# Performance work log

Hardware: AMD Instinct MI355X
Metric: run time of the kernel (lower is better)

The kernel has to match this reference:

```python
import jax, jax.numpy as jnp
import numpy as np

NUM_HEADS = 12
LN_EPS = 1e-5


def _layernorm(t, w, b):
    # LayerNorm over last dim (head_dim), biased variance as in torch
    mu = jnp.mean(t, axis=-1, keepdims=True)
    var = jnp.mean(jnp.square(t - mu), axis=-1, keepdims=True)
    return (t - mu) * jax.lax.rsqrt(var + LN_EPS) * w + b


def _apply_rope(t, cos, sin):
    # t: [B, H, S, D]; cos/sin: [S, D//2]; interleaved complex pairs (torch view_as_complex)
    tr = t[..., 0::2]
    ti = t[..., 1::2]
    c = cos[None, None, :, :]
    s = sin[None, None, :, :]
    out_r = tr * c - ti * s
    out_i = tr * s + ti * c
    return jnp.stack([out_r, out_i], axis=-1).reshape(t.shape)


def setup_inputs() -> dict:
    key = jax.random.key(0)
    ks = jax.random.split(key, 6)
    B, N, C = 16, 1024, 768
    H = NUM_HEADS
    D = C // H  # 64
    P, L = 1, 32
    rot_len = N - P - L  # 991
    x = jax.random.normal(ks[0], (B, N, C), dtype=jnp.float32)
    # rotary frequencies (llama-style)
    inv_freq = 1.0 / (10000.0 ** (np.arange(0, D, 2, dtype=np.float32) / D))
    angles = np.arange(rot_len, dtype=np.float32)[:, None] * inv_freq[None, :]
    cos = jnp.asarray(np.cos(angles))
    sin = jnp.asarray(np.sin(angles))
    # parameters (qkv_bias=False, qk_norm=True)
    w_qkv = jax.random.normal(ks[1], (C, 3 * C), dtype=jnp.float32) * (C ** -0.5)
    q_ln_w = jnp.ones((D,), jnp.float32)
    q_ln_b = jnp.zeros((D,), jnp.float32)
    k_ln_w = jnp.ones((D,), jnp.float32)
    k_ln_b = jnp.zeros((D,), jnp.float32)
    w_proj = jax.random.normal(ks[2], (C, C), dtype=jnp.float32) * (C ** -0.5)
    b_proj = jnp.zeros((C,), jnp.float32)
    return {
        "x": x, "cos": cos, "sin": sin,
        "w_qkv": w_qkv,
        "q_ln_w": q_ln_w, "q_ln_b": q_ln_b,
        "k_ln_w": k_ln_w, "k_ln_b": k_ln_b,
        "w_proj": w_proj, "b_proj": b_proj,
        "num_prefix_tokens": 1, "num_latent_tokens": 32,
    }


def reference(x, cos, sin, w_qkv, q_ln_w, q_ln_b, k_ln_w, k_ln_b, w_proj, b_proj,
              num_prefix_tokens, num_latent_tokens):
    B, N, C = x.shape
    H = NUM_HEADS
    D = C // H
    P, L = num_prefix_tokens, num_latent_tokens
    scale = D ** -0.5

    qkv = (x @ w_qkv).reshape(B, N, 3, H, D)
    qkv = jnp.transpose(qkv, (2, 0, 3, 1, 4))  # [3, B, H, N, D]
    q, k, v = qkv[0], qkv[1], qkv[2]

    q = _layernorm(q, q_ln_w, q_ln_b)
    k = _layernorm(k, k_ln_w, k_ln_b)

    # partial RoPE: only the middle [P : N-L] tokens are rotated
    q_rot = _apply_rope(q[:, :, P:N - L], cos, sin)
    k_rot = _apply_rope(k[:, :, P:N - L], cos, sin)
    q = jnp.concatenate([q[:, :, :P], q_rot, q[:, :, N - L:]], axis=2)
    k = jnp.concatenate([k[:, :, :P], k_rot, k[:, :, N - L:]], axis=2)

    attn = jnp.einsum("bhqd,bhkd->bhqk", q * scale, k)
    attn = jax.nn.softmax(attn, axis=-1)
    out = jnp.einsum("bhqk,bhkd->bhqd", attn, v)
    out = jnp.transpose(out, (0, 2, 1, 3)).reshape(B, N, C)
    return out @ w_proj + b_proj
```

## Files before the change

kernel.cpp:

```cpp
#include <hip/hip_runtime.h>
#include <hip/hip_bf16.h>

typedef __attribute__((ext_vector_type(8))) short v8s;
typedef __attribute__((ext_vector_type(4))) short v4s;
typedef __attribute__((ext_vector_type(4))) float f32x4;

__device__ __forceinline__ float bf2f(short s){
  unsigned u = ((unsigned)(unsigned short)s) << 16;
  float f; __builtin_memcpy(&f, &u, 4); return f;
}
__device__ __forceinline__ short f2bf(float f){
  unsigned u; __builtin_memcpy(&u, &f, 4);
  unsigned r = (u + 0x7FFFu + ((u >> 16) & 1u)) >> 16;
  return (short)r;
}

__global__ __launch_bounds__(256) void k_cast8(const float* __restrict__ in,
                                               short* __restrict__ out, long n){
  long i = ((long)blockIdx.x * 256 + threadIdx.x) * 8;
  long stride = (long)gridDim.x * 256 * 8;
  for (; i < n; i += stride){
    float4 a = *(const float4*)(in + i);
    float4 b = *(const float4*)(in + i + 4);
    v8s v;
    v[0]=f2bf(a.x); v[1]=f2bf(a.y); v[2]=f2bf(a.z); v[3]=f2bf(a.w);
    v[4]=f2bf(b.x); v[5]=f2bf(b.y); v[6]=f2bf(b.z); v[7]=f2bf(b.w);
    *(v8s*)(out + i) = v;
  }
}

__global__ __launch_bounds__(256) void k_tcast(const float* __restrict__ in,
                                               short* __restrict__ out, int R, int Cc){
  __shared__ float T[32][33];
  int tx = threadIdx.x & 31, ty = threadIdx.x >> 5;
  int r0 = blockIdx.x * 32, c0 = blockIdx.y * 32;
  #pragma unroll
  for (int p = 0; p < 4; p++){
    int r = ty + p*8;
    T[r][tx] = in[(long)(r0 + r)*Cc + c0 + tx];
  }
  __syncthreads();
  #pragma unroll
  for (int p = 0; p < 4; p++){
    int r = ty + p*8;
    out[(long)(c0 + r)*R + r0 + tx] = f2bf(T[tx][r]);
  }
}

template<int OUT_MODE>
__global__ __launch_bounds__(256) void k_gemm(const short* __restrict__ A,
                                              const short* __restrict__ Bt,
                                              void* __restrict__ Cout,
                                              const float* __restrict__ bias,
                                              int M, int N, int K){
  __shared__ short As[128][72];
  __shared__ short Bs[128][72];
  int row0 = blockIdx.x * 128, col0 = blockIdx.y * 128;
  int t = threadIdx.x;
  int lane = t & 63, w = t >> 6;
  int g = lane >> 4, r16 = lane & 15;
  int wr = w >> 1, wc = w & 1;
  f32x4 acc[4][4];
  #pragma unroll
  for (int mi = 0; mi < 4; mi++)
    #pragma unroll
    for (int ni = 0; ni < 4; ni++)
      acc[mi][ni] = (f32x4){0.f,0.f,0.f,0.f};

  for (int kt = 0; kt < K; kt += 64){
    #pragma unroll
    for (int p = 0; p < 4; p++){
      int idx = t + p*256;
      int rr = idx >> 3, vc = idx & 7;
      *(v8s*)&As[rr][vc*8] = *(const v8s*)&A[(long)(row0 + rr)*K + kt + vc*8];
    }
    #pragma unroll
    for (int p = 0; p < 4; p++){
      int idx = t + p*256;
      int rr = idx >> 3, vc = idx & 7;
      *(v8s*)&Bs[rr][vc*8] = *(const v8s*)&Bt[(long)(col0 + rr)*K + kt + vc*8];
    }
    __syncthreads();
    #pragma unroll
    for (int ks = 0; ks < 2; ks++){
      v8s af[4], bfr[4];
      #pragma unroll
      for (int mi = 0; mi < 4; mi++)
        af[mi] = *(const v8s*)&As[wr*64 + mi*16 + r16][ks*32 + g*8];
      #pragma unroll
      for (int ni = 0; ni < 4; ni++)
        bfr[ni] = *(const v8s*)&Bs[wc*64 + ni*16 + r16][ks*32 + g*8];
      #pragma unroll
      for (int mi = 0; mi < 4; mi++)
        #pragma unroll
        for (int ni = 0; ni < 4; ni++)
          acc[mi][ni] = __builtin_amdgcn_mfma_f32_16x16x32_bf16(af[mi], bfr[ni], acc[mi][ni], 0, 0, 0);
    }
    __syncthreads();
  }
  #pragma unroll
  for (int mi = 0; mi < 4; mi++)
    #pragma unroll
    for (int ni = 0; ni < 4; ni++){
      int rbase = row0 + wr*64 + mi*16 + g*4;
      int cc = col0 + wc*64 + ni*16 + r16;
      #pragma unroll
      for (int j = 0; j < 4; j++){
        float v = acc[mi][ni][j];
        if (OUT_MODE == 0)
          ((short*)Cout)[(long)(rbase + j)*N + cc] = f2bf(v);
        else
          ((float*)Cout)[(long)(rbase + j)*N + cc] = v + bias[cc];
      }
    }
}

__global__ __launch_bounds__(256) void k_lnrope(const short* __restrict__ QKV,
     const float* __restrict__ cosT, const float* __restrict__ sinT,
     const float* __restrict__ qw, const float* __restrict__ qb,
     const float* __restrict__ kw, const float* __restrict__ kb,
     short* __restrict__ Qb, short* __restrict__ Kb, short* __restrict__ Vt){
  __shared__ short Vs[64][72];
  int blk = blockIdx.x;
  int ntile = blk & 15, h = (blk >> 4) % 12, b = blk / 192;
  int t = threadIdx.x;
  int tl = t >> 2, ch = t & 3;
  int n = ntile*64 + tl;
  long row = (long)(b*1024 + n) * 2304;
  int d0 = ch * 16;
  long outrow = ((long)(b*12 + h)*1024 + n) * 64;

  #pragma unroll
  for (int sel = 0; sel < 2; sel++){
    const short* src = &QKV[row + sel*768 + h*64 + d0];
    float f[16];
    v8s a0 = *(const v8s*)src;
    v8s a1 = *(const v8s*)(src + 8);
    #pragma unroll
    for (int i = 0; i < 8; i++){ f[i] = bf2f(a0[i]); f[8+i] = bf2f(a1[i]); }
    float s1 = 0.f, s2 = 0.f;
    #pragma unroll
    for (int i = 0; i < 16; i++){ s1 += f[i]; s2 += f[i]*f[i]; }
    s1 += __shfl_xor(s1, 1); s2 += __shfl_xor(s2, 1);
    s1 += __shfl_xor(s1, 2); s2 += __shfl_xor(s2, 2);
    float mu = s1 * (1.0f/64.0f);
    float var = s2 * (1.0f/64.0f) - mu*mu;
    float rs = rsqrtf(var + 1e-5f);
    const float* wp = sel ? kw : qw;
    const float* bp = sel ? kb : qb;
    #pragma unroll
    for (int i = 0; i < 16; i++) f[i] = (f[i] - mu)*rs*wp[d0+i] + bp[d0+i];
    if (n >= 1 && n < 992){
      int pos = n - 1;
      const float* cp = &cosT[pos*32 + ch*8];
      const float* sp = &sinT[pos*32 + ch*8];
      #pragma unroll
      for (int i = 0; i < 8; i++){
        float c = cp[i], s = sp[i];
        float tr = f[2*i], ti = f[2*i+1];
        f[2*i]   = tr*c - ti*s;
        f[2*i+1] = tr*s + ti*c;
      }
    }
    if (sel == 0){
      #pragma unroll
      for (int i = 0; i < 16; i++) f[i] *= 0.125f;
    }
    v8s o0, o1;
    #pragma unroll
    for (int i = 0; i < 8; i++){ o0[i] = f2bf(f[i]); o1[i] = f2bf(f[8+i]); }
    short* dst = sel ? &Kb[outrow + d0] : &Qb[outrow + d0];
    *(v8s*)dst = o0;
    *(v8s*)(dst + 8) = o1;
  }
  {
    const short* vsrc = &QKV[row + 1536 + h*64 + d0];
    *(v8s*)&Vs[tl][d0]     = *(const v8s*)vsrc;
    *(v8s*)&Vs[tl][d0 + 8] = *(const v8s*)(vsrc + 8);
  }
  __syncthreads();
  {
    int d = tl, nch = ch;
    v8s o0, o1;
    #pragma unroll
    for (int i = 0; i < 8; i++){ o0[i] = Vs[nch*16 + i][d]; o1[i] = Vs[nch*16 + 8 + i][d]; }
    long vrow = ((long)(b*12 + h)*64 + d)*1024 + ntile*64 + nch*16;
    *(v8s*)&Vt[vrow]     = o0;
    *(v8s*)&Vt[vrow + 8] = o1;
  }
}

__global__ __launch_bounds__(256) void k_attn(const short* __restrict__ Qb,
                                              const short* __restrict__ Kb,
                                              const short* __restrict__ Vt,
                                              short* __restrict__ O){
  __shared__ short Ks[64][72];
  __shared__ short Vts[64][72];
  int blk = blockIdx.x;
  int qt = blk & 15, h = (blk >> 4) % 12, b = blk / 192;
  long bh = b*12 + h;
  int t = threadIdx.x, lane = t & 63, w = t >> 6;
  int g = lane >> 4, r16 = lane & 15;
  int q0 = qt*64 + w*16;

  v8s bq[2];
  #pragma unroll
  for (int tt = 0; tt < 2; tt++)
    bq[tt] = *(const v8s*)&Qb[(bh*1024 + q0 + r16)*64 + tt*32 + g*8];

  f32x4 oacc[4];
  #pragma unroll
  for (int t2 = 0; t2 < 4; t2++) oacc[t2] = (f32x4){0.f,0.f,0.f,0.f};
  float m_run = -1e30f, l_run = 0.f;

  for (int kt = 0; kt < 1024; kt += 64){
    #pragma unroll
    for (int p = 0; p < 2; p++){
      int idx = t + p*256;
      int rr = idx >> 3, vc = idx & 7;
      *(v8s*)&Ks[rr][vc*8]  = *(const v8s*)&Kb[(bh*1024 + kt + rr)*64 + vc*8];
      *(v8s*)&Vts[rr][vc*8] = *(const v8s*)&Vt[(bh*64 + rr)*1024 + kt + vc*8];
    }
    __syncthreads();

    f32x4 sacc[4];
    #pragma unroll
    for (int f = 0; f < 4; f++) sacc[f] = (f32x4){0.f,0.f,0.f,0.f};
    #pragma unroll
    for (int tt = 0; tt < 2; tt++){
      #pragma unroll
      for (int f = 0; f < 4; f++){
        v8s ak = *(const v8s*)&Ks[f*16 + r16][tt*32 + g*8];
        sacc[f] = __builtin_amdgcn_mfma_f32_16x16x32_bf16(ak, bq[tt], sacc[f], 0, 0, 0);
      }
    }
    float mt = -1e30f;
    #pragma unroll
    for (int f = 0; f < 4; f++)
      #pragma unroll
      for (int j = 0; j < 4; j++) mt = fmaxf(mt, sacc[f][j]);
    mt = fmaxf(mt, __shfl_xor(mt, 16));
    mt = fmaxf(mt, __shfl_xor(mt, 32));
    float m_new = fmaxf(m_run, mt);
    float alpha = __expf(m_run - m_new);
    float p[4][4];
    float lsum = 0.f;
    #pragma unroll
    for (int f = 0; f < 4; f++)
      #pragma unroll
      for (int j = 0; j < 4; j++){
        p[f][j] = __expf(sacc[f][j] - m_new);
        lsum += p[f][j];
      }
    lsum += __shfl_xor(lsum, 16);
    lsum += __shfl_xor(lsum, 32);
    l_run = l_run*alpha + lsum;
    m_run = m_new;
    float aj4[4];
    #pragma unroll
    for (int j = 0; j < 4; j++) aj4[j] = __shfl(alpha, 4*g + j, 64);
    #pragma unroll
    for (int t2 = 0; t2 < 4; t2++)
      #pragma unroll
      for (int j = 0; j < 4; j++) oacc[t2][j] *= aj4[j];

    v8s pa[4];
    #pragma unroll
    for (int f = 0; f < 4; f++){
      #pragma unroll
      for (int j = 0; j < 4; j++) pa[f][j] = f2bf(p[f][j]);
      #pragma unroll
      for (int j = 4; j < 8; j++) pa[f][j] = 0;
    }
    #pragma unroll
    for (int t2 = 0; t2 < 4; t2++)
      #pragma unroll
      for (int f = 0; f < 4; f++){
        v4s v4 = *(const v4s*)&Vts[t2*16 + r16][f*16 + g*4];
        v8s bv;
        bv[0]=v4[0]; bv[1]=v4[1]; bv[2]=v4[2]; bv[3]=v4[3];
        bv[4]=0; bv[5]=0; bv[6]=0; bv[7]=0;
        oacc[t2] = __builtin_amdgcn_mfma_f32_16x16x32_bf16(pa[f], bv, oacc[t2], 0, 0, 0);
      }
    __syncthreads();
  }
  float linv = 1.0f / l_run;
  float lj[4];
  #pragma unroll
  for (int j = 0; j < 4; j++) lj[j] = __shfl(linv, 4*g + j, 64);
  #pragma unroll
  for (int t2 = 0; t2 < 4; t2++)
    #pragma unroll
    for (int j = 0; j < 4; j++){
      float v = oacc[t2][j] * lj[j];
      O[((long)b*1024 + q0 + 4*g + j)*768 + h*64 + t2*16 + r16] = f2bf(v);
    }
}

extern "C" void kernel_launch(void* const* d_in, const int* in_sizes, int n_in,
                              void* d_out, int out_size, void* d_ws, size_t ws_size,
                              hipStream_t stream) {
  const float* x      = (const float*)d_in[0];
  const float* cosT   = (const float*)d_in[1];
  const float* sinT   = (const float*)d_in[2];
  const float* w_qkv  = (const float*)d_in[3];
  const float* q_ln_w = (const float*)d_in[4];
  const float* q_ln_b = (const float*)d_in[5];
  const float* k_ln_w = (const float*)d_in[6];
  const float* k_ln_b = (const float*)d_in[7];
  const float* w_proj = (const float*)d_in[8];
  const float* b_proj = (const float*)d_in[9];

  char* ws = (char*)d_ws;
  short* Xb       = (short*)(ws);
  short* Wqkv_bt  = (short*)(ws + 25165824);
  short* Wproj_bt = (short*)(ws + 28704768);
  short* QKV      = (short*)(ws + 29884416);
  short* Qb       = (short*)(ws + 105381888);
  short* Kb       = (short*)(ws + 130547712);
  short* Vt       = (short*)(ws + 155713536);
  short* O        = (short*)(ws + 180879360);

  k_cast8<<<6144, 256, 0, stream>>>(x, Xb, 12582912L);
  k_tcast<<<dim3(24, 72), 256, 0, stream>>>(w_qkv, Wqkv_bt, 768, 2304);
  k_tcast<<<dim3(24, 24), 256, 0, stream>>>(w_proj, Wproj_bt, 768, 768);
  k_gemm<0><<<dim3(128, 18), 256, 0, stream>>>(Xb, Wqkv_bt, QKV, nullptr, 16384, 2304, 768);
  k_lnrope<<<3072, 256, 0, stream>>>(QKV, cosT, sinT, q_ln_w, q_ln_b, k_ln_w, k_ln_b, Qb, Kb, Vt);
  k_attn<<<3072, 256, 0, stream>>>(Qb, Kb, Vt, O);
  k_gemm<1><<<dim3(128, 6), 256, 0, stream>>>(O, Wproj_bt, d_out, b_proj, 16384, 768, 768);
}
```

Before: 420.2 us.

## Use direct global-to-LDS loads with XOR swizzle, exp2 softmax, larger attention blocks

GEMM and attention tiles are now loaded with global_load_lds straight into unpadded LDS. An XOR swizzle on the column index avoids bank conflicts, and the loads skip the register round trip. The Q scale folds in log2(e) so the softmax can use exp2f. Attention blocks grow to 512 threads with 128 queries each, so every K/V tile is reused by twice as many queries. The swizzle has to match the per-wave LDS destination layout of global_load_lds exactly, and the larger blocks may reduce occupancy.

```diff
diff --git a/kernel.cpp b/kernel.cpp
--- a/kernel.cpp
+++ b/kernel.cpp
@@ -13,6 +13,11 @@
   unsigned u; __builtin_memcpy(&u, &f, 4);
   unsigned r = (u + 0x7FFFu + ((u >> 16) & 1u)) >> 16;
   return (short)r;
+}
+
+__device__ __forceinline__ void gload16(const void* g, void* l){
+  __builtin_amdgcn_global_load_lds((const __attribute__((address_space(1))) void*)g,
+                                   (__attribute__((address_space(3))) void*)l, 16, 0, 0);
 }
 
 __global__ __launch_bounds__(256) void k_cast8(const float* __restrict__ in,
@@ -53,13 +58,16 @@
                                               void* __restrict__ Cout,
                                               const float* __restrict__ bias,
                                               int M, int N, int K){
-  __shared__ short As[128][72];
-  __shared__ short Bs[128][72];
+  __shared__ short As[128*64];
+  __shared__ short Bs[128*64];
   int row0 = blockIdx.x * 128, col0 = blockIdx.y * 128;
   int t = threadIdx.x;
   int lane = t & 63, w = t >> 6;
   int g = lane >> 4, r16 = lane & 15;
   int wr = w >> 1, wc = w & 1;
+  int rsw = (r16 & 7) << 3;
+  int srow = t >> 3;
+  int scol = ((t & 7) * 8) ^ ((srow & 7) << 3);
   f32x4 acc[4][4];
   #pragma unroll
   for (int mi = 0; mi < 4; mi++)
@@ -70,15 +78,13 @@
   for (int kt = 0; kt < K; kt += 64){
     #pragma unroll
     for (int p = 0; p < 4; p++){
-      int idx = t + p*256;
-      int rr = idx >> 3, vc = idx & 7;
-      *(v8s*)&As[rr][vc*8] = *(const v8s*)&A[(long)(row0 + rr)*K + kt + vc*8];
+      int rr = p*32 + srow;
+      gload16(&A[(long)(row0 + rr)*K + kt + scol], &As[(p*256 + w*64)*8]);
     }
     #pragma unroll
     for (int p = 0; p < 4; p++){
-      int idx = t + p*256;
-      int rr = idx >> 3, vc = idx & 7;
-      *(v8s*)&Bs[rr][vc*8] = *(const v8s*)&Bt[(long)(col0 + rr)*K + kt + vc*8];
+      int rr = p*32 + srow;
+      gload16(&Bt[(long)(col0 + rr)*K + kt + scol], &Bs[(p*256 + w*64)*8]);
     }
     __syncthreads();
     #pragma unroll
@@ -86,10 +92,10 @@
       v8s af[4], bfr[4];
       #pragma unroll
       for (int mi = 0; mi < 4; mi++)
-        af[mi] = *(const v8s*)&As[wr*64 + mi*16 + r16][ks*32 + g*8];
+        af[mi] = *(const v8s*)&As[(wr*64 + mi*16 + r16)*64 + ((ks*32 + g*8) ^ rsw)];
       #pragma unroll
       for (int ni = 0; ni < 4; ni++)
-        bfr[ni] = *(const v8s*)&Bs[wc*64 + ni*16 + r16][ks*32 + g*8];
+        bfr[ni] = *(const v8s*)&Bs[(wc*64 + ni*16 + r16)*64 + ((ks*32 + g*8) ^ rsw)];
       #pragma unroll
       for (int mi = 0; mi < 4; mi++)
         #pragma unroll
@@ -164,7 +170,7 @@
     }
     if (sel == 0){
       #pragma unroll
-      for (int i = 0; i < 16; i++) f[i] *= 0.125f;
+      for (int i = 0; i < 16; i++) f[i] *= 0.18033688011112042f;
     }
     v8s o0, o1;
     #pragma unroll
@@ -190,18 +196,26 @@
   }
 }
 
-__global__ __launch_bounds__(256) void k_attn(const short* __restrict__ Qb,
+__global__ __launch_bounds__(512) void k_attn(const short* __restrict__ Qb,
                                               const short* __restrict__ Kb,
                                               const short* __restrict__ Vt,
                                               short* __restrict__ O){
-  __shared__ short Ks[64][72];
-  __shared__ short Vts[64][72];
+  __shared__ short Ks[64*64];
+  __shared__ short Vts[64*64];
   int blk = blockIdx.x;
-  int qt = blk & 15, h = (blk >> 4) % 12, b = blk / 192;
+  int qt = blk & 7, h = (blk >> 3) % 12, b = blk / 96;
   long bh = b*12 + h;
   int t = threadIdx.x, lane = t & 63, w = t >> 6;
   int g = lane >> 4, r16 = lane & 15;
-  int q0 = qt*64 + w*16;
+  int rsw = (r16 & 7) << 3;
+  int q0 = qt*128 + w*16;
+
+  int srow = t >> 3;
+  int scol = ((t & 7) * 8) ^ ((srow & 7) << 3);
+  const short* Ksrc = &Kb[(bh*1024 + srow)*64 + scol];
+  const short* Vsrc = &Vt[(bh*64 + srow)*1024 + scol];
+  short* KsBase  = &Ks[w*512];
+  short* VtsBase = &Vts[w*512];
 
   v8s bq[2];
   #pragma unroll
@@ -214,13 +228,8 @@
   float m_run = -1e30f, l_run = 0.f;
 
   for (int kt = 0; kt < 1024; kt += 64){
-    #pragma unroll
-    for (int p = 0; p < 2; p++){
-      int idx = t + p*256;
-      int rr = idx >> 3, vc = idx & 7;
-      *(v8s*)&Ks[rr][vc*8]  = *(const v8s*)&Kb[(bh*1024 + kt + rr)*64 + vc*8];
-      *(v8s*)&Vts[rr][vc*8] = *(const v8s*)&Vt[(bh*64 + rr)*1024 + kt + vc*8];
-    }
+    gload16(Ksrc + kt*64, KsBase);
+    gload16(Vsrc + kt,    VtsBase);
     __syncthreads();
 
     f32x4 sacc[4];
@@ -230,7 +239,7 @@
     for (int tt = 0; tt < 2; tt++){
       #pragma unroll
       for (int f = 0; f < 4; f++){
-        v8s ak = *(const v8s*)&Ks[f*16 + r16][tt*32 + g*8];
+        v8s ak = *(const v8s*)&Ks[(f*16 + r16)*64 + ((tt*32 + g*8) ^ rsw)];
         sacc[f] = __builtin_amdgcn_mfma_f32_16x16x32_bf16(ak, bq[tt], sacc[f], 0, 0, 0);
       }
     }
@@ -242,14 +251,14 @@
     mt = fmaxf(mt, __shfl_xor(mt, 16));
     mt = fmaxf(mt, __shfl_xor(mt, 32));
     float m_new = fmaxf(m_run, mt);
-    float alpha = __expf(m_run - m_new);
+    float alpha = exp2f(m_run - m_new);
     float p[4][4];
     float lsum = 0.f;
     #pragma unroll
     for (int f = 0; f < 4; f++)
       #pragma unroll
       for (int j = 0; j < 4; j++){
-        p[f][j] = __expf(sacc[f][j] - m_new);
+        p[f][j] = exp2f(sacc[f][j] - m_new);
         lsum += p[f][j];
       }
     lsum += __shfl_xor(lsum, 16);
@@ -276,7 +285,7 @@
     for (int t2 = 0; t2 < 4; t2++)
       #pragma unroll
       for (int f = 0; f < 4; f++){
-        v4s v4 = *(const v4s*)&Vts[t2*16 + r16][f*16 + g*4];
+        v4s v4 = *(const v4s*)&Vts[(t2*16 + r16)*64 + ((f*16 + g*4) ^ rsw)];
         v8s bv;
         bv[0]=v4[0]; bv[1]=v4[1]; bv[2]=v4[2]; bv[3]=v4[3];
         bv[4]=0; bv[5]=0; bv[6]=0; bv[7]=0;
@@ -326,6 +335,6 @@
   k_tcast<<<dim3(24, 24), 256, 0, stream>>>(w_proj, Wproj_bt, 768, 768);
   k_gemm<0><<<dim3(128, 18), 256, 0, stream>>>(Xb, Wqkv_bt, QKV, nullptr, 16384, 2304, 768);
   k_lnrope<<<3072, 256, 0, stream>>>(QKV, cosT, sinT, q_ln_w, q_ln_b, k_ln_w, k_ln_b, Qb, Kb, Vt);
-  k_attn<<<3072, 256, 0, stream>>>(Qb, Kb, Vt, O);
+  k_attn<<<1536, 512, 0, stream>>>(Qb, Kb, Vt, O);
   k_gemm<1><<<dim3(128, 6), 256, 0, stream>>>(O, Wproj_bt, d_out, b_proj, 16384, 768, 768);
 }
```

New measurement: 393.0 us. 6.5% less time.
